# Optimization experiments

Hardware: AMD Instinct MI355X
Metric: run time of the kernel (lower is better)

Reference implementation:

```python
import jax, jax.numpy as jnp
import numpy as np
from jax import lax

WORD_DIM = 300
VOCAB = 50000
PATTERN_LEN = 6
NUM_DIAGS = 3
DOC_LEN = 500000


def setup_inputs() -> dict:
    key = jax.random.key(0)
    k1, k2, k3, k4 = jax.random.split(key, 4)
    embeddings = jax.random.normal(k1, (WORD_DIM, VOCAB), dtype=jnp.float32)
    diags = jax.random.normal(k2, (NUM_DIAGS, WORD_DIM, PATTERN_LEN), dtype=jnp.float32)
    # original normalize(): each row (length pattern_length) of each diag divided by its norm
    diags = diags / jnp.linalg.norm(diags, axis=-1, keepdims=True)
    bias = jax.random.normal(k3, (NUM_DIAGS, PATTERN_LEN), dtype=jnp.float32)
    doc = jax.random.randint(k4, (DOC_LEN,), 0, VOCAB, dtype=jnp.int64)
    return {"embeddings": embeddings, "diags": diags, "bias": bias, "doc": doc}


def reference(embeddings, diags, bias, doc):
    P = diags.shape[-1]
    dtype = embeddings.dtype
    # Gather word vectors for the whole doc: (T, D)
    emb_doc = embeddings[:, doc].T
    # Only the "one forward" diagonal (index 1) is used by forward().
    # gate[t] = sigmoid(x_t @ diags[1] + bias[1])  -> (T, P)
    gate = jax.nn.sigmoid(jnp.einsum("td,dp->tp", emb_doc, diags[1]) + bias[1])
    start = jnp.zeros((P,), dtype=dtype).at[0].set(1.0)

    def step(carry, g):
        hidden, score = carry
        # hidden_new = start + [0, hidden[:-1] * gate[:-1]]
        shifted = jnp.concatenate([jnp.zeros((1,), dtype=dtype), hidden[:-1] * g[:-1]])
        hidden_new = start + shifted
        return (hidden_new, score + hidden_new[-1]), None

    (hidden, score), _ = lax.scan(step, (start, jnp.zeros((), dtype=dtype)), gate)
    return score
```

## Files before the change

kernel.cpp:

```cpp
#include <hip/hip_runtime.h>


#define WORD_DIM 300
#define VOCAB    50000
#define PLEN     6
#define DOC_LEN  500000

#define GROUPS   6
#define GSIZE    128
#define DCHUNK   50
#define K1_BLOCK (GROUPS * GSIZE)

__global__ __launch_bounds__(K1_BLOCK) void proj_sig_fused(
    const float* __restrict__ emb,
    const float* __restrict__ diags,
    const float* __restrict__ bias,
    float* __restrict__ sig)
{
    __shared__ float wl[WORD_DIM * 5];
    __shared__ float part[GROUPS - 1][GSIZE][10];
    const int tid = threadIdx.x;
    for (int i = tid; i < WORD_DIM * 5; i += K1_BLOCK) {
        int d = i / 5, p = i % 5;
        wl[i] = diags[WORD_DIM * PLEN + d * PLEN + p];
    }
    __syncthreads();

    const int g  = tid / GSIZE;
    const int u  = tid % GSIZE;
    const int v2 = blockIdx.x * (2 * GSIZE) + u * 2;
    const int d0 = g * DCHUNK;

    float a[10] = {0.f, 0.f, 0.f, 0.f, 0.f, 0.f, 0.f, 0.f, 0.f, 0.f};
    if (v2 < VOCAB) {
        const float* __restrict__ col = emb + (size_t)d0 * VOCAB + v2;
        #pragma unroll 10
        for (int dd = 0; dd < DCHUNK; ++dd) {
            float2 x = *reinterpret_cast<const float2*>(&col[(size_t)dd * VOCAB]);
            const float* w = &wl[(d0 + dd) * 5];
            a[0] += x.x * w[0]; a[1] += x.x * w[1]; a[2] += x.x * w[2];
            a[3] += x.x * w[3]; a[4] += x.x * w[4];
            a[5] += x.y * w[0]; a[6] += x.y * w[1]; a[7] += x.y * w[2];
            a[8] += x.y * w[3]; a[9] += x.y * w[4];
        }
    }
    if (g > 0) {
        #pragma unroll
        for (int k = 0; k < 10; ++k) part[g - 1][u][k] = a[k];
    }
    __syncthreads();
    if (g == 0 && v2 < VOCAB) {
        #pragma unroll
        for (int k = 0; k < 10; ++k) {
            float s = a[k];
            #pragma unroll
            for (int q = 0; q < GROUPS - 1; ++q) s += part[q][u][k];
            a[k] = s;
        }
        float* r0 = &sig[(size_t)v2 * 8];
        float* r1 = &sig[(size_t)(v2 + 1) * 8];
        #pragma unroll
        for (int p = 0; p < 5; ++p) {
            float b = bias[PLEN + p];
            r0[p] = 1.f / (1.f + __expf(-(a[p]     + b)));
            r1[p] = 1.f / (1.f + __expf(-(a[5 + p] + b)));
        }
    }
}

#define K2_BLOCK 1024
#define K2_TOK   (K2_BLOCK + 4)

__global__ __launch_bounds__(K2_BLOCK) void score_kernel(
    const int* __restrict__ doc,
    const float* __restrict__ sig,
    float* __restrict__ partials)
{
    __shared__ float srow[5][K2_TOK];
    const int tid  = threadIdx.x;
    const int base = blockIdx.x * K2_BLOCK + 4;
    for (int i = tid; i < K2_TOK; i += K2_BLOCK) {
        int tok_t = base - 4 + i;
        if (tok_t < DOC_LEN) {
            const float* row = &sig[(size_t)doc[tok_t] * 8];
            float4 r4 = *reinterpret_cast<const float4*>(row);
            srow[0][i] = r4.x; srow[1][i] = r4.y; srow[2][i] = r4.z; srow[3][i] = r4.w;
            srow[4][i] = row[4];
        }
    }
    __syncthreads();

    const int t = base + tid;
    float prod = 0.f;
    if (t < DOC_LEN) {
        prod = srow[0][tid] * srow[1][tid + 1] * srow[2][tid + 2]
             * srow[3][tid + 3] * srow[4][tid + 4];
    }
    #pragma unroll
    for (int off = 32; off > 0; off >>= 1)
        prod += __shfl_down(prod, off, 64);
    __shared__ float wsum[K2_BLOCK / 64];
    const int lane = tid & 63;
    const int wid  = tid >> 6;
    if (lane == 0) wsum[wid] = prod;
    __syncthreads();
    if (tid == 0) {
        float s = 0.f;
        #pragma unroll
        for (int w = 0; w < K2_BLOCK / 64; ++w) s += wsum[w];
        partials[blockIdx.x] = s;
    }
}

__global__ __launch_bounds__(512) void reduce_kernel(
    const float* __restrict__ partials, int n, float* __restrict__ out)
{
    float s = 0.f;
    for (int i = threadIdx.x; i < n; i += 512) s += partials[i];
    #pragma unroll
    for (int off = 32; off > 0; off >>= 1)
        s += __shfl_down(s, off, 64);
    __shared__ float wsum[8];
    const int lane = threadIdx.x & 63;
    const int wid  = threadIdx.x >> 6;
    if (lane == 0) wsum[wid] = s;
    __syncthreads();
    if (threadIdx.x == 0) {
        float t = 0.f;
        #pragma unroll
        for (int w = 0; w < 8; ++w) t += wsum[w];
        out[0] = t;
    }
}

extern "C" void kernel_launch(void* const* d_in, const int* in_sizes, int n_in,
                              void* d_out, int out_size, void* d_ws, size_t ws_size,
                              hipStream_t stream) {
    const float* emb   = (const float*)d_in[0];
    const float* diags = (const float*)d_in[1];
    const float* bias  = (const float*)d_in[2];
    const int*   doc   = (const int*)d_in[3];
    float* out = (float*)d_out;

    float* ws = (float*)d_ws;
    float* sig   = ws;
    float* bpart = sig + (size_t)VOCAB * 8;

    const int blocks1 = (VOCAB + 2 * GSIZE - 1) / (2 * GSIZE);
    const int nwin    = DOC_LEN - 4;
    const int blocks2 = (nwin + K2_BLOCK - 1) / K2_BLOCK;

    proj_sig_fused<<<blocks1, K1_BLOCK, 0, stream>>>(emb, diags, bias, sig);
    score_kernel<<<blocks2, K2_BLOCK, 0, stream>>>(doc, sig, bpart);
    reduce_kernel<<<1, 512, 0, stream>>>(bpart, blocks2, out);
}
```

Measured before the change: 26.05 us.

## Fuse final reduction into score kernel via last-block atomic counter; retile projection

Removes the separate reduce kernel launch. Each score block atomically increments a counter, and the last block to finish sums all partials. The projection kernel is also retiled to 100 vocab words per block, using 64-thread groups and more blocks (500 instead of 196) to spread the vocab sweep across more CUs. The counter is reset by the first projection block, and the change relies on one block of 1024 threads being able to cover all 489 partials.

```diff
diff --git a/kernel.cpp b/kernel.cpp
--- a/kernel.cpp
+++ b/kernel.cpp
@@ -7,32 +7,35 @@
 #define DOC_LEN  500000
 
 #define GROUPS   6
-#define GSIZE    128
 #define DCHUNK   50
-#define K1_BLOCK (GROUPS * GSIZE)
+#define K1_BLOCK (GROUPS * 64)
+#define VBLK     100
 
 __global__ __launch_bounds__(K1_BLOCK) void proj_sig_fused(
     const float* __restrict__ emb,
     const float* __restrict__ diags,
     const float* __restrict__ bias,
-    float* __restrict__ sig)
+    float* __restrict__ sig,
+    unsigned int* __restrict__ ctr)
 {
     __shared__ float wl[WORD_DIM * 5];
-    __shared__ float part[GROUPS - 1][GSIZE][10];
+    __shared__ float part[GROUPS - 1][VBLK / 2][10];
     const int tid = threadIdx.x;
+    if (blockIdx.x == 0 && tid == 0) *ctr = 0u;
     for (int i = tid; i < WORD_DIM * 5; i += K1_BLOCK) {
         int d = i / 5, p = i % 5;
         wl[i] = diags[WORD_DIM * PLEN + d * PLEN + p];
     }
     __syncthreads();
 
-    const int g  = tid / GSIZE;
-    const int u  = tid % GSIZE;
-    const int v2 = blockIdx.x * (2 * GSIZE) + u * 2;
-    const int d0 = g * DCHUNK;
+    const int g   = tid >> 6;
+    const int u   = tid & 63;
+    const bool act = (u < VBLK / 2);
+    const int v2  = blockIdx.x * VBLK + u * 2;
+    const int d0  = g * DCHUNK;
 
     float a[10] = {0.f, 0.f, 0.f, 0.f, 0.f, 0.f, 0.f, 0.f, 0.f, 0.f};
-    if (v2 < VOCAB) {
+    if (act) {
         const float* __restrict__ col = emb + (size_t)d0 * VOCAB + v2;
         #pragma unroll 10
         for (int dd = 0; dd < DCHUNK; ++dd) {
@@ -44,12 +47,12 @@
             a[8] += x.y * w[3]; a[9] += x.y * w[4];
         }
     }
-    if (g > 0) {
+    if (g > 0 && act) {
         #pragma unroll
         for (int k = 0; k < 10; ++k) part[g - 1][u][k] = a[k];
     }
     __syncthreads();
-    if (g == 0 && v2 < VOCAB) {
+    if (g == 0 && act) {
         #pragma unroll
         for (int k = 0; k < 10; ++k) {
             float s = a[k];
@@ -70,11 +73,14 @@
 
 #define K2_BLOCK 1024
 #define K2_TOK   (K2_BLOCK + 4)
+#define K2_GRID  ((DOC_LEN - 4 + K2_BLOCK - 1) / K2_BLOCK)
 
 __global__ __launch_bounds__(K2_BLOCK) void score_kernel(
     const int* __restrict__ doc,
     const float* __restrict__ sig,
-    float* __restrict__ partials)
+    float* __restrict__ partials,
+    unsigned int* __restrict__ ctr,
+    float* __restrict__ out)
 {
     __shared__ float srow[5][K2_TOK];
     const int tid  = threadIdx.x;
@@ -104,32 +110,32 @@
     const int wid  = tid >> 6;
     if (lane == 0) wsum[wid] = prod;
     __syncthreads();
+
+    __shared__ bool is_last;
     if (tid == 0) {
         float s = 0.f;
         #pragma unroll
         for (int w = 0; w < K2_BLOCK / 64; ++w) s += wsum[w];
         partials[blockIdx.x] = s;
+        __threadfence();
+        unsigned int old = atomicAdd(ctr, 1u);
+        is_last = (old == K2_GRID - 1);
     }
-}
+    __syncthreads();
+    if (!is_last) return;
 
-__global__ __launch_bounds__(512) void reduce_kernel(
-    const float* __restrict__ partials, int n, float* __restrict__ out)
-{
-    float s = 0.f;
-    for (int i = threadIdx.x; i < n; i += 512) s += partials[i];
+    __threadfence();
+    float s = (tid < K2_GRID) ? partials[tid] : 0.f;
     #pragma unroll
     for (int off = 32; off > 0; off >>= 1)
         s += __shfl_down(s, off, 64);
-    __shared__ float wsum[8];
-    const int lane = threadIdx.x & 63;
-    const int wid  = threadIdx.x >> 6;
     if (lane == 0) wsum[wid] = s;
     __syncthreads();
-    if (threadIdx.x == 0) {
-        float t = 0.f;
+    if (tid == 0) {
+        float tot = 0.f;
         #pragma unroll
-        for (int w = 0; w < 8; ++w) t += wsum[w];
-        out[0] = t;
+        for (int w = 0; w < K2_BLOCK / 64; ++w) tot += wsum[w];
+        out[0] = tot;
     }
 }
 
@@ -145,12 +151,10 @@
     float* ws = (float*)d_ws;
     float* sig   = ws;
     float* bpart = sig + (size_t)VOCAB * 8;
+    unsigned int* ctr = (unsigned int*)(bpart + K2_GRID);
 
-    const int blocks1 = (VOCAB + 2 * GSIZE - 1) / (2 * GSIZE);
-    const int nwin    = DOC_LEN - 4;
-    const int blocks2 = (nwin + K2_BLOCK - 1) / K2_BLOCK;
+    const int blocks1 = VOCAB / VBLK;
 
-    proj_sig_fused<<<blocks1, K1_BLOCK, 0, stream>>>(emb, diags, bias, sig);
-    score_kernel<<<blocks2, K2_BLOCK, 0, stream>>>(doc, sig, bpart);
-    reduce_kernel<<<1, 512, 0, stream>>>(bpart, blocks2, out);
+    proj_sig_fused<<<blocks1, K1_BLOCK, 0, stream>>>(emb, diags, bias, sig, ctr);
+    score_kernel<<<K2_GRID, K2_BLOCK, 0, stream>>>(doc, sig, bpart, ctr, out);
 }
```

After: 37.96 us. 1.46x slower.
